# Performance work log

Measured on AMD Instinct MI355X. Metric: run time of the kernel, lower is better.

Reference implementation:

```python
import jax, jax.numpy as jnp
import numpy as np

D = 1024
B, S = 4, 2048

def setup_inputs() -> dict:
    key = jax.random.key(0)
    ks = jax.random.split(key, 4)
    scale = 1.0 / np.sqrt(D)
    return {
        "x": jax.random.normal(ks[0], (B, S, D), dtype=jnp.float32),
        "Wq": jax.random.normal(ks[1], (D, D), dtype=jnp.float32) * scale,
        "bq": jnp.zeros((D,), jnp.float32),
        "Wk": jax.random.normal(ks[2], (D, D), dtype=jnp.float32) * scale,
        "bk": jnp.zeros((D,), jnp.float32),
        "Wv": jax.random.normal(ks[3], (D, D), dtype=jnp.float32) * scale,
        "bv": jnp.zeros((D,), jnp.float32),
    }

def reference(x, Wq, bq, Wk, bk, Wv, bv):
    # torch Linear: y = x @ W.T + b
    Q = jnp.einsum('bsd,ed->bse', x, Wq) + bq
    K = jnp.einsum('bsd,ed->bse', x, Wk) + bk
    V = jnp.einsum('bsd,ed->bse', x, Wv) + bv
    # NOTE: original scales by sqrt(K.shape[1]) == sqrt(seq_len), kept faithfully
    dk = K.shape[1]
    logits = jnp.einsum('bqd,bkd->bqk', Q, K) / jnp.sqrt(jnp.asarray(dk, Q.dtype))
    att = jax.nn.softmax(logits, axis=-1)
    return jnp.einsum('bqk,bkd->bqd', att, V)
```

## Files before the change

kernel.cpp:

```cpp
#include <hip/hip_runtime.h>


typedef unsigned short u16;
typedef unsigned int u32;
typedef __bf16 bf16x8 __attribute__((ext_vector_type(8)));
typedef float floatx4 __attribute__((ext_vector_type(4)));

__device__ __forceinline__ u16 f2bf(float f) {
    u32 u = __float_as_uint(f);
    u += 0x7fffu + ((u >> 16) & 1u);
    return (u16)(u >> 16);
}

__device__ __forceinline__ void g2lds16(const void* g, void* l) {
    __builtin_amdgcn_global_load_lds(
        (const __attribute__((address_space(1))) unsigned int*)g,
        (__attribute__((address_space(3))) unsigned int*)l,
        16, 0, 0);
}

__global__ __launch_bounds__(256)
void cvt_f32_bf16(const float* __restrict__ in, u16* __restrict__ out, int n4) {
    int i = blockIdx.x * 256 + threadIdx.x;
    if (i >= n4) return;
    float4 v = ((const float4*)in)[i];
    ushort4 o;
    o.x = f2bf(v.x); o.y = f2bf(v.y); o.z = f2bf(v.z); o.w = f2bf(v.w);
    ((ushort4*)out)[i] = o;
}

template<int MODE>
__global__ __launch_bounds__(256)
void gemm_bt(const u16* __restrict__ A, const u16* __restrict__ B,
             void* __restrict__ Out, const float* __restrict__ bias,
             float scale, int M, int N, int K,
             long long sAz, long long sBz, long long sOz)
{
    __shared__ u16 ldsA[2][128 * 64];
    __shared__ u16 ldsB[2][128 * 64];

    const int tid   = threadIdx.x;
    const int lane  = tid & 63;
    const int wv    = tid >> 6;
    const int wm    = (wv >> 1) * 64;
    const int wn    = (wv & 1) * 64;
    const int lhalf = lane & 15;
    const int quad  = lane >> 4;

    const size_t bz = blockIdx.z;
    A += bz * (size_t)sAz;
    B += bz * (size_t)sBz;

    int tm, tn;
    {
        const int ntn = gridDim.x, ntm = gridDim.y;
        const int lin = blockIdx.y * ntn + blockIdx.x;
        const int GM = 4;
        const int width = GM * ntn;
        const int group = lin / width;
        const int first = group * GM;
        const int gsz   = (ntm - first) < GM ? (ntm - first) : GM;
        const int rem   = lin - group * width;
        tm = first + rem % gsz;
        tn = rem / gsz;
    }
    const int m0 = tm * 128;
    const int n0 = tn * 128;

    const int r8 = lane >> 3;
    const int gc = (lane & 7) ^ r8;
    const u16* pa = A + (size_t)(m0 + wv * 32 + r8) * K + gc * 8;
    const u16* pb = B + (size_t)(n0 + wv * 32 + r8) * K + gc * 8;
    const int lofs = wv * 2048;

    floatx4 zero = {0.f, 0.f, 0.f, 0.f};
    floatx4 acc[4][4];
#pragma unroll
    for (int i = 0; i < 4; ++i)
#pragma unroll
        for (int j = 0; j < 4; ++j) acc[i][j] = zero;

    const int swz = lhalf & 7;

#pragma unroll
    for (int j = 0; j < 4; ++j) {
        g2lds16(pa + (size_t)(j * 8) * K, &ldsA[0][lofs + j * 512]);
        g2lds16(pb + (size_t)(j * 8) * K, &ldsB[0][lofs + j * 512]);
    }
    pa += 64; pb += 64;

    int buf = 0;
    for (int k0 = 0; k0 < K; k0 += 64) {
        __syncthreads();
        if (k0 + 64 < K) {
#pragma unroll
            for (int j = 0; j < 4; ++j) {
                g2lds16(pa + (size_t)(j * 8) * K, &ldsA[buf ^ 1][lofs + j * 512]);
                g2lds16(pb + (size_t)(j * 8) * K, &ldsB[buf ^ 1][lofs + j * 512]);
            }
            pa += 64; pb += 64;
        }

        const u16* lA = ldsA[buf];
        const u16* lB = ldsB[buf];
#pragma unroll
        for (int ks = 0; ks < 2; ++ks) {
            bf16x8 af[4], bfv[4];
            const int c = ks * 4 + quad;
            const int p = c ^ swz;
#pragma unroll
            for (int i = 0; i < 4; ++i)
                af[i] = *(const bf16x8*)(lA + (wm + i * 16 + lhalf) * 64 + p * 8);
#pragma unroll
            for (int j = 0; j < 4; ++j)
                bfv[j] = *(const bf16x8*)(lB + (wn + j * 16 + lhalf) * 64 + p * 8);
#pragma unroll
            for (int i = 0; i < 4; ++i)
#pragma unroll
                for (int j = 0; j < 4; ++j)
                    acc[i][j] = __builtin_amdgcn_mfma_f32_16x16x32_bf16(
                        af[i], bfv[j], acc[i][j], 0, 0, 0);
        }
        buf ^= 1;
    }

#pragma unroll
    for (int i = 0; i < 4; ++i) {
        const int mb = m0 + wm + i * 16 + quad * 4;
#pragma unroll
        for (int j = 0; j < 4; ++j) {
            const int n = n0 + wn + j * 16 + lhalf;
            const float bb = bias ? bias[n] : 0.f;
#pragma unroll
            for (int r = 0; r < 4; ++r) {
                const int m = mb + r;
                const float v = acc[i][j][r] * scale + bb;
                if (MODE == 2) {
                    ((float*)Out)[bz * (size_t)sOz + (size_t)m * N + n] = v;
                } else if (MODE == 0) {
                    ((u16*)Out)[bz * (size_t)sOz + (size_t)m * N + n] = f2bf(v);
                } else {
                    ((u16*)Out)[bz * (size_t)sOz + (size_t)n * M + m] = f2bf(v);
                }
            }
        }
    }
}

__global__ __launch_bounds__(256)
void softmax_rows(u16* __restrict__ S)
{
    const int tid = threadIdx.x;
    u16* row = S + (size_t)blockIdx.x * 2048;
    uint4 v = ((const uint4*)row)[tid];
    float x[8];
    x[0] = __uint_as_float(v.x << 16); x[1] = __uint_as_float(v.x & 0xffff0000u);
    x[2] = __uint_as_float(v.y << 16); x[3] = __uint_as_float(v.y & 0xffff0000u);
    x[4] = __uint_as_float(v.z << 16); x[5] = __uint_as_float(v.z & 0xffff0000u);
    x[6] = __uint_as_float(v.w << 16); x[7] = __uint_as_float(v.w & 0xffff0000u);

    float mx = x[0];
#pragma unroll
    for (int i = 1; i < 8; ++i) mx = fmaxf(mx, x[i]);
#pragma unroll
    for (int off = 32; off > 0; off >>= 1) mx = fmaxf(mx, __shfl_xor(mx, off, 64));

    __shared__ float sm[4], ss[4];
    if ((tid & 63) == 0) sm[tid >> 6] = mx;
    __syncthreads();
    mx = fmaxf(fmaxf(sm[0], sm[1]), fmaxf(sm[2], sm[3]));

    float e[8];
    float s = 0.f;
#pragma unroll
    for (int i = 0; i < 8; ++i) { e[i] = __expf(x[i] - mx); s += e[i]; }
#pragma unroll
    for (int off = 32; off > 0; off >>= 1) s += __shfl_xor(s, off, 64);
    if ((tid & 63) == 0) ss[tid >> 6] = s;
    __syncthreads();
    s = (ss[0] + ss[1]) + (ss[2] + ss[3]);

    const float inv = 1.f / s;
    uint4 o;
    o.x = (u32)f2bf(e[0] * inv) | ((u32)f2bf(e[1] * inv) << 16);
    o.y = (u32)f2bf(e[2] * inv) | ((u32)f2bf(e[3] * inv) << 16);
    o.z = (u32)f2bf(e[4] * inv) | ((u32)f2bf(e[5] * inv) << 16);
    o.w = (u32)f2bf(e[6] * inv) | ((u32)f2bf(e[7] * inv) << 16);
    ((uint4*)row)[tid] = o;
}

extern "C" void kernel_launch(void* const* d_in, const int* in_sizes, int n_in,
                              void* d_out, int out_size, void* d_ws, size_t ws_size,
                              hipStream_t stream)
{
    const float* x  = (const float*)d_in[0];
    const float* Wq = (const float*)d_in[1];
    const float* bq = (const float*)d_in[2];
    const float* Wk = (const float*)d_in[3];
    const float* bk = (const float*)d_in[4];
    const float* Wv = (const float*)d_in[5];
    const float* bv = (const float*)d_in[6];
    float* out = (float*)d_out;

    const int B = 4, S = 2048, D = 1024;
    const long long SD = (long long)S * D;
    const long long SS = (long long)S * S;
    const long long BSD = (long long)B * SD;
    const long long DD = (long long)D * D;

    u16* xb  = (u16*)d_ws;
    u16* wqb = xb  + BSD;
    u16* wkb = wqb + DD;
    u16* wvb = wkb + DD;
    u16* Qb  = wvb + DD;
    u16* Kb  = Qb  + BSD;
    u16* Vt  = Kb  + BSD;
    u16* Sc  = Vt  + BSD;

    cvt_f32_bf16<<<dim3((int)(BSD / 4 / 256)), 256, 0, stream>>>(x,  xb,  (int)(BSD / 4));
    cvt_f32_bf16<<<dim3((int)(DD  / 4 / 256)), 256, 0, stream>>>(Wq, wqb, (int)(DD / 4));
    cvt_f32_bf16<<<dim3((int)(DD  / 4 / 256)), 256, 0, stream>>>(Wk, wkb, (int)(DD / 4));
    cvt_f32_bf16<<<dim3((int)(DD  / 4 / 256)), 256, 0, stream>>>(Wv, wvb, (int)(DD / 4));

    gemm_bt<0><<<dim3(D / 128, (B * S) / 128, 1), 256, 0, stream>>>(
        xb, wqb, Qb, bq, 1.f, B * S, D, D, 0, 0, 0);
    gemm_bt<0><<<dim3(D / 128, (B * S) / 128, 1), 256, 0, stream>>>(
        xb, wkb, Kb, bk, 1.f, B * S, D, D, 0, 0, 0);
    gemm_bt<1><<<dim3(D / 128, S / 128, B), 256, 0, stream>>>(
        xb, wvb, Vt, bv, 1.f, S, D, D, SD, 0, SD);

    const float sc = 0.022097086912079608f;
    gemm_bt<0><<<dim3(S / 128, S / 128, B), 256, 0, stream>>>(
        Qb, Kb, Sc, nullptr, sc, S, S, D, SD, SD, SS);

    softmax_rows<<<dim3(B * S), 256, 0, stream>>>(Sc);

    gemm_bt<2><<<dim3(D / 128, S / 128, B), 256, 0, stream>>>(
        Sc, Vt, out, nullptr, 1.f, S, D, S, SS, SD, SD);
}
```

Before: 271.8 us.

## Fuse QKV projection into one GEMM, merge conversions, enlarge GEMM tiles to 256x256

Merges the four f32-to-bf16 conversion launches into a single kernel. The three projection GEMMs become one GEMM against a concatenated weight matrix, and the epilogue routes each column range to Q, K or transposed V with its bias. All GEMMs move to 256x256 tiles with 512 threads and 4x8 MFMA accumulators per wave, so each loaded tile is reused across more output. The aim is fewer launches and more data reuse, at the cost of higher register and LDS use per block (64KB LDS) and fewer blocks for the smaller GEMMs.

```diff
diff --git a/kernel.cpp b/kernel.cpp
--- a/kernel.cpp
+++ b/kernel.cpp
@@ -20,30 +20,51 @@
 }
 
 __global__ __launch_bounds__(256)
-void cvt_f32_bf16(const float* __restrict__ in, u16* __restrict__ out, int n4) {
+void cvt_all(const float* __restrict__ x, const float* __restrict__ Wq,
+             const float* __restrict__ Wk, const float* __restrict__ Wv,
+             u16* __restrict__ xb, u16* __restrict__ wall)
+{
+    const int NX = 2097152;
+    const int NW = 262144;
     int i = blockIdx.x * 256 + threadIdx.x;
-    if (i >= n4) return;
-    float4 v = ((const float4*)in)[i];
+    const float* src;
+    u16* dst;
+    int idx;
+    if (i < NX) { src = x; dst = xb; idx = i; }
+    else {
+        int j = i - NX;
+        dst = wall; idx = j;
+        src = (j < NW) ? Wq : (j < 2 * NW) ? Wk : Wv;
+        int jj = (j < NW) ? j : (j < 2 * NW) ? (j - NW) : (j - 2 * NW);
+        float4 v = ((const float4*)src)[jj];
+        ushort4 o;
+        o.x = f2bf(v.x); o.y = f2bf(v.y); o.z = f2bf(v.z); o.w = f2bf(v.w);
+        ((ushort4*)dst)[idx] = o;
+        return;
+    }
+    float4 v = ((const float4*)src)[idx];
     ushort4 o;
     o.x = f2bf(v.x); o.y = f2bf(v.y); o.z = f2bf(v.z); o.w = f2bf(v.w);
-    ((ushort4*)out)[i] = o;
+    ((ushort4*)dst)[idx] = o;
 }
 
 template<int MODE>
-__global__ __launch_bounds__(256)
-void gemm_bt(const u16* __restrict__ A, const u16* __restrict__ B,
-             void* __restrict__ Out, const float* __restrict__ bias,
-             float scale, int M, int N, int K,
-             long long sAz, long long sBz, long long sOz)
-{
-    __shared__ u16 ldsA[2][128 * 64];
-    __shared__ u16 ldsB[2][128 * 64];
+__global__ __launch_bounds__(512, 2)
+void gemm_big(const u16* __restrict__ A, const u16* __restrict__ B,
+              void* __restrict__ Out, const float* __restrict__ bias,
+              float scale, int M, int N, int K,
+              long long sAz, long long sBz, long long sOz,
+              void* __restrict__ Out2, void* __restrict__ Out3,
+              const float* __restrict__ bias2, const float* __restrict__ bias3)
+{
+    __shared__ u16 ldsA[2][256 * 64];
+    __shared__ u16 ldsB[2][256 * 64];
 
     const int tid   = threadIdx.x;
     const int lane  = tid & 63;
     const int wv    = tid >> 6;
     const int wm    = (wv >> 1) * 64;
-    const int wn    = (wv & 1) * 64;
+    const int wn    = (wv & 1) * 128;
     const int lhalf = lane & 15;
     const int quad  = lane >> 4;
 
@@ -64,28 +85,28 @@
         tm = first + rem % gsz;
         tn = rem / gsz;
     }
-    const int m0 = tm * 128;
-    const int n0 = tn * 128;
+    const int m0 = tm * 256;
+    const int n0 = tn * 256;
 
     const int r8 = lane >> 3;
     const int gc = (lane & 7) ^ r8;
-    const u16* pa = A + (size_t)(m0 + wv * 32 + r8) * K + gc * 8;
-    const u16* pb = B + (size_t)(n0 + wv * 32 + r8) * K + gc * 8;
-    const int lofs = wv * 2048;
+    const u16* pa = A + (size_t)(m0 + 8 * wv + r8) * K + gc * 8;
+    const u16* pb = B + (size_t)(n0 + 8 * wv + r8) * K + gc * 8;
+    const int lbase = wv * 512;
 
     floatx4 zero = {0.f, 0.f, 0.f, 0.f};
-    floatx4 acc[4][4];
+    floatx4 acc[4][8];
 #pragma unroll
     for (int i = 0; i < 4; ++i)
 #pragma unroll
-        for (int j = 0; j < 4; ++j) acc[i][j] = zero;
+        for (int j = 0; j < 8; ++j) acc[i][j] = zero;
 
     const int swz = lhalf & 7;
 
 #pragma unroll
     for (int j = 0; j < 4; ++j) {
-        g2lds16(pa + (size_t)(j * 8) * K, &ldsA[0][lofs + j * 512]);
-        g2lds16(pb + (size_t)(j * 8) * K, &ldsB[0][lofs + j * 512]);
+        g2lds16(pa + (size_t)(64 * j) * K, &ldsA[0][lbase + j * 4096]);
+        g2lds16(pb + (size_t)(64 * j) * K, &ldsB[0][lbase + j * 4096]);
     }
     pa += 64; pb += 64;
 
@@ -95,8 +116,8 @@
         if (k0 + 64 < K) {
 #pragma unroll
             for (int j = 0; j < 4; ++j) {
-                g2lds16(pa + (size_t)(j * 8) * K, &ldsA[buf ^ 1][lofs + j * 512]);
-                g2lds16(pb + (size_t)(j * 8) * K, &ldsB[buf ^ 1][lofs + j * 512]);
+                g2lds16(pa + (size_t)(64 * j) * K, &ldsA[buf ^ 1][lbase + j * 4096]);
+                g2lds16(pb + (size_t)(64 * j) * K, &ldsB[buf ^ 1][lbase + j * 4096]);
             }
             pa += 64; pb += 64;
         }
@@ -105,19 +126,19 @@
         const u16* lB = ldsB[buf];
 #pragma unroll
         for (int ks = 0; ks < 2; ++ks) {
-            bf16x8 af[4], bfv[4];
             const int c = ks * 4 + quad;
             const int p = c ^ swz;
+            bf16x8 af[4], bfv[8];
 #pragma unroll
             for (int i = 0; i < 4; ++i)
                 af[i] = *(const bf16x8*)(lA + (wm + i * 16 + lhalf) * 64 + p * 8);
 #pragma unroll
-            for (int j = 0; j < 4; ++j)
+            for (int j = 0; j < 8; ++j)
                 bfv[j] = *(const bf16x8*)(lB + (wn + j * 16 + lhalf) * 64 + p * 8);
 #pragma unroll
             for (int i = 0; i < 4; ++i)
 #pragma unroll
-                for (int j = 0; j < 4; ++j)
+                for (int j = 0; j < 8; ++j)
                     acc[i][j] = __builtin_amdgcn_mfma_f32_16x16x32_bf16(
                         af[i], bfv[j], acc[i][j], 0, 0, 0);
         }
@@ -128,19 +149,43 @@
     for (int i = 0; i < 4; ++i) {
         const int mb = m0 + wm + i * 16 + quad * 4;
 #pragma unroll
-        for (int j = 0; j < 4; ++j) {
+        for (int j = 0; j < 8; ++j) {
             const int n = n0 + wn + j * 16 + lhalf;
-            const float bb = bias ? bias[n] : 0.f;
-#pragma unroll
-            for (int r = 0; r < 4; ++r) {
-                const int m = mb + r;
-                const float v = acc[i][j][r] * scale + bb;
-                if (MODE == 2) {
-                    ((float*)Out)[bz * (size_t)sOz + (size_t)m * N + n] = v;
-                } else if (MODE == 0) {
-                    ((u16*)Out)[bz * (size_t)sOz + (size_t)m * N + n] = f2bf(v);
+            if (MODE == 0) {
+#pragma unroll
+                for (int r = 0; r < 4; ++r)
+                    ((u16*)Out)[bz * (size_t)sOz + (size_t)(mb + r) * N + n] =
+                        f2bf(acc[i][j][r] * scale);
+            } else if (MODE == 2) {
+#pragma unroll
+                for (int r = 0; r < 4; ++r)
+                    ((float*)Out)[bz * (size_t)sOz + (size_t)(mb + r) * N + n] =
+                        acc[i][j][r] * scale;
+            } else {
+                if (n < 1024) {
+                    const float bb = bias[n];
+#pragma unroll
+                    for (int r = 0; r < 4; ++r)
+                        ((u16*)Out)[(size_t)(mb + r) * 1024 + n] =
+                            f2bf(acc[i][j][r] + bb);
+                } else if (n < 2048) {
+                    const float bb = bias2[n - 1024];
+#pragma unroll
+                    for (int r = 0; r < 4; ++r)
+                        ((u16*)Out2)[(size_t)(mb + r) * 1024 + (n - 1024)] =
+                            f2bf(acc[i][j][r] + bb);
                 } else {
-                    ((u16*)Out)[bz * (size_t)sOz + (size_t)n * M + m] = f2bf(v);
+                    const int d = n - 2048;
+                    const float bb = bias3[d];
+                    const int b = mb >> 11;
+                    const int s0 = mb & 2047;
+                    ushort4 w;
+                    w.x = f2bf(acc[i][j][0] + bb);
+                    w.y = f2bf(acc[i][j][1] + bb);
+                    w.z = f2bf(acc[i][j][2] + bb);
+                    w.w = f2bf(acc[i][j][3] + bb);
+                    *(ushort4*)((u16*)Out3 + (size_t)b * 2097152 +
+                                (size_t)d * 2048 + s0) = w;
                 }
             }
         }
@@ -208,33 +253,26 @@
     const long long BSD = (long long)B * SD;
     const long long DD = (long long)D * D;
 
-    u16* xb  = (u16*)d_ws;
-    u16* wqb = xb  + BSD;
-    u16* wkb = wqb + DD;
-    u16* wvb = wkb + DD;
-    u16* Qb  = wvb + DD;
-    u16* Kb  = Qb  + BSD;
-    u16* Vt  = Kb  + BSD;
-    u16* Sc  = Vt  + BSD;
-
-    cvt_f32_bf16<<<dim3((int)(BSD / 4 / 256)), 256, 0, stream>>>(x,  xb,  (int)(BSD / 4));
-    cvt_f32_bf16<<<dim3((int)(DD  / 4 / 256)), 256, 0, stream>>>(Wq, wqb, (int)(DD / 4));
-    cvt_f32_bf16<<<dim3((int)(DD  / 4 / 256)), 256, 0, stream>>>(Wk, wkb, (int)(DD / 4));
-    cvt_f32_bf16<<<dim3((int)(DD  / 4 / 256)), 256, 0, stream>>>(Wv, wvb, (int)(DD / 4));
-
-    gemm_bt<0><<<dim3(D / 128, (B * S) / 128, 1), 256, 0, stream>>>(
-        xb, wqb, Qb, bq, 1.f, B * S, D, D, 0, 0, 0);
-    gemm_bt<0><<<dim3(D / 128, (B * S) / 128, 1), 256, 0, stream>>>(
-        xb, wkb, Kb, bk, 1.f, B * S, D, D, 0, 0, 0);
-    gemm_bt<1><<<dim3(D / 128, S / 128, B), 256, 0, stream>>>(
-        xb, wvb, Vt, bv, 1.f, S, D, D, SD, 0, SD);
+    u16* xb   = (u16*)d_ws;
+    u16* wall = xb   + BSD;
+    u16* Qb   = wall + 3 * DD;
+    u16* Kb   = Qb   + BSD;
+    u16* Vt   = Kb   + BSD;
+    u16* Sc   = Vt   + BSD;
+
+    cvt_all<<<dim3(11264), 256, 0, stream>>>(x, Wq, Wk, Wv, xb, wall);
+
+    gemm_big<3><<<dim3(3 * D / 256, (B * S) / 256, 1), 512, 0, stream>>>(
+        xb, wall, Qb, bq, 1.f, B * S, 3 * D, D, 0, 0, 0, Kb, Vt, bk, bv);
 
     const float sc = 0.022097086912079608f;
-    gemm_bt<0><<<dim3(S / 128, S / 128, B), 256, 0, stream>>>(
-        Qb, Kb, Sc, nullptr, sc, S, S, D, SD, SD, SS);
+    gemm_big<0><<<dim3(S / 256, S / 256, B), 512, 0, stream>>>(
+        Qb, Kb, Sc, nullptr, sc, S, S, D, SD, SD, SS,
+        nullptr, nullptr, nullptr, nullptr);
 
     softmax_rows<<<dim3(B * S), 256, 0, stream>>>(Sc);
 
-    gemm_bt<2><<<dim3(D / 128, S / 128, B), 256, 0, stream>>>(
-        Sc, Vt, out, nullptr, 1.f, S, D, S, SS, SD, SD);
-}
+    gemm_big<2><<<dim3(D / 256, S / 256, B), 512, 0, stream>>>(
+        Sc, Vt, out, nullptr, 1.f, S, D, S, SS, SD, SD,
+        nullptr, nullptr, nullptr, nullptr);
+}
```

After: 294.3 us. +8.3%, slower.
